# Kernel tuning notes

Measured on AMD Instinct MI355X. Metric: run time of the kernel, lower is better.

## Reference

```python
import jax, jax.numpy as jnp
import numpy as np

B, T, HID = 2, 2048, 2048
N_HEADS, N_KV, HEAD_DIM = 32, 8, 64
THETA = 10000.0
SCALE = HEAD_DIM ** -0.5
STEPS = 2  # entries already in cache before this call (step_idx)


def _rope_cos_sin(pos):
    # pos: [B, T] int -> cos/sin [B, T, HEAD_DIM]
    inv_freq = 1.0 / (THETA ** (jnp.arange(0, HEAD_DIM, 2, dtype=jnp.float32) / HEAD_DIM))
    freqs = pos.astype(jnp.float32)[..., None] * inv_freq  # [B,T,D/2]
    emb = jnp.concatenate([freqs, freqs], axis=-1)
    return jnp.cos(emb), jnp.sin(emb)


def _rotate_half(x):
    x1, x2 = jnp.split(x, 2, axis=-1)
    return jnp.concatenate([-x2, x1], axis=-1)


def setup_inputs() -> dict:
    key = jax.random.key(0)
    ks = jax.random.split(key, 8)
    combined_states = jax.random.normal(ks[0], (B, T, 2 * HID), dtype=jnp.float32)
    # additive causal mask: 0 on/below diagonal, large negative above
    causal = jnp.tril(jnp.ones((T, T), dtype=bool))
    attention_mask = jnp.where(causal, 0.0, -1e9).astype(jnp.float32)[None, None].repeat(B, axis=0)
    position_ids = jnp.broadcast_to(jnp.arange(T, dtype=jnp.int32), (B, T))
    prev_k = jax.random.normal(ks[1], (STEPS, B, N_HEADS, T, HEAD_DIM), dtype=jnp.float32)
    prev_v = jax.random.normal(ks[2], (STEPS, B, N_HEADS, T, HEAD_DIM), dtype=jnp.float32)
    Wq = 0.02 * jax.random.normal(ks[3], (2 * HID, N_HEADS * HEAD_DIM), dtype=jnp.float32)
    Wk = 0.02 * jax.random.normal(ks[4], (2 * HID, N_KV * HEAD_DIM), dtype=jnp.float32)
    Wv = 0.02 * jax.random.normal(ks[5], (2 * HID, N_KV * HEAD_DIM), dtype=jnp.float32)
    Wo = 0.02 * jax.random.normal(ks[6], (N_HEADS * HEAD_DIM, HID), dtype=jnp.float32)
    return {"combined_states": combined_states, "attention_mask": attention_mask,
            "position_ids": position_ids, "prev_k": prev_k, "prev_v": prev_v,
            "Wq": Wq, "Wk": Wk, "Wv": Wv, "Wo": Wo}


def reference(combined_states, attention_mask, position_ids, prev_k, prev_v, Wq, Wk, Wv, Wo):
    b, t, _ = combined_states.shape
    step_idx = prev_k.shape[0]  # len(cache_k) before append
    groups = N_HEADS // N_KV

    # fused QKV projection -> [B, H, T, D]
    q = (combined_states @ Wq).reshape(b, t, N_HEADS, HEAD_DIM).transpose(0, 2, 1, 3)
    k = (combined_states @ Wk).reshape(b, t, N_KV, HEAD_DIM).transpose(0, 2, 1, 3)
    v = (combined_states @ Wv).reshape(b, t, N_KV, HEAD_DIM).transpose(0, 2, 1, 3)

    # RoPE with phase shift by step_idx
    cos, sin = _rope_cos_sin(position_ids + step_idx)
    cos, sin = cos[:, None], sin[:, None]  # [B,1,T,D]
    q = q * cos + _rotate_half(q) * sin
    k = k * cos + _rotate_half(k) * sin

    # GQA expansion (repeat_interleave over head dim)
    k = jnp.repeat(k, groups, axis=1)
    v = jnp.repeat(v, groups, axis=1)

    # cache after append: [prev_0, prev_1, ..., k_new]; k0 = cache[0], later = cache[1:]
    k0, v0 = prev_k[0], prev_v[0]
    later_k = jnp.concatenate([prev_k[1:], k[None]], axis=0)  # [S, B, H, T, D], S = step_idx
    later_v = jnp.concatenate([prev_v[1:], v[None]], axis=0)

    # block attention over K_0 plus growing diagonal terms
    attn = jnp.einsum('bhtd,bhsd->bhts', q, k0) * SCALE + attention_mask  # [B,H,T,T]
    diag = jnp.einsum('bhtd,sbhtd->bhts', q, later_k) * SCALE             # [B,H,T,S]
    logits = jnp.concatenate([attn, diag], axis=-1)                        # [B,H,T,T+S]
    probs = jax.nn.softmax(logits.astype(jnp.float32), axis=-1).astype(q.dtype)

    out = jnp.einsum('bhts,bhsd->bhtd', probs[..., :t], v0)
    out = out + jnp.einsum('bhts,sbhtd->bhtd', probs[..., t:], later_v)
    out = out.transpose(0, 2, 1, 3).reshape(b, t, N_HEADS * HEAD_DIM)
    return out @ Wo
```

## Files before the change

### kernel.cpp

```cpp
#include <hip/hip_runtime.h>

#define B_    2
#define T_    2048
#define HID_  2048
#define NH_   32
#define NKV_  8
#define HD_   64
#define STEPS_ 2
#define SCALE_ 0.125f
#define CSC_  0.18033688011112042f

typedef float   f32x4  __attribute__((ext_vector_type(4)));
typedef __bf16  bf16x8 __attribute__((ext_vector_type(8)));
typedef unsigned short u16x8 __attribute__((ext_vector_type(8)));

__device__ __forceinline__ unsigned short f2bf(float f) {
  unsigned int u = __builtin_bit_cast(unsigned int, f);
  u = (u + 0x7fffu + ((u >> 16) & 1u)) >> 16;
  return (unsigned short)u;
}
__device__ __forceinline__ float bf2f(unsigned short h) {
  unsigned int u = ((unsigned int)h) << 16;
  return __builtin_bit_cast(float, u);
}
__device__ __forceinline__ bf16x8 frag_ld(const unsigned short* p) {
  u16x8 v = *(const u16x8*)p;
  return __builtin_bit_cast(bf16x8, v);
}
__device__ __forceinline__ f32x4 mfma16(bf16x8 a, bf16x8 b, f32x4 c) {
  return __builtin_amdgcn_mfma_f32_16x16x32_bf16(a, b, c, 0, 0, 0);
}
__device__ __forceinline__ void async_cp16(const void* g, void* l) {
  __builtin_amdgcn_global_load_lds(
      (const __attribute__((address_space(1))) void*)g,
      (__attribute__((address_space(3))) void*)l, 16, 0, 0);
}
__device__ __forceinline__ unsigned int cvtpk_bf16(float lo, float hi) {
  unsigned int r;
  asm("v_cvt_pk_bf16_f32 %0, %1, %2" : "=v"(r) : "v"(lo), "v"(hi));
  return r;
}

__global__ __launch_bounds__(256) void convert_bf16(const float* __restrict__ in,
                                                    unsigned short* __restrict__ out,
                                                    int n4) {
  int idx = blockIdx.x * 256 + threadIdx.x;
  if (idx < n4) {
    float4 v = ((const float4*)in)[idx];
    ushort4 o;
    o.x = f2bf(v.x); o.y = f2bf(v.y); o.z = f2bf(v.z); o.w = f2bf(v.w);
    ((ushort4*)out)[idx] = o;
  }
}

__global__ __launch_bounds__(256) void transpose_f32_bf16_ld(const float* __restrict__ in,
                                                             unsigned short* __restrict__ out,
                                                             int K, int N, int ldo) {
  __shared__ float tile[64][65];
  int n0 = blockIdx.x * 64, k0 = blockIdx.y * 64;
  int c = threadIdx.x & 63, w = threadIdx.x >> 6;
#pragma unroll
  for (int i = 0; i < 16; i++) {
    int r = w * 16 + i;
    tile[r][c] = in[(size_t)(k0 + r) * N + n0 + c];
  }
  __syncthreads();
#pragma unroll
  for (int i = 0; i < 16; i++) {
    int rr = w * 16 + i;
    out[(size_t)(n0 + rr) * ldo + k0 + c] = f2bf(tile[c][rr]);
  }
}

__global__ __launch_bounds__(256) void transpose_v0(const float* __restrict__ v0,
                                                    unsigned short* __restrict__ v0t) {
  __shared__ float tile[64][65];
  int s0 = blockIdx.x * 64;
  int bh = blockIdx.y;
  const float* src = v0 + (size_t)bh * T_ * HD_;
  unsigned short* dst = v0t + (size_t)bh * HD_ * T_;
  int c = threadIdx.x & 63, w = threadIdx.x >> 6;
#pragma unroll
  for (int i = 0; i < 16; i++) {
    int r = w * 16 + i;
    tile[r][c] = src[(size_t)(s0 + r) * HD_ + c];
  }
  __syncthreads();
#pragma unroll
  for (int i = 0; i < 16; i++) {
    int rr = w * 16 + i;
    dst[(size_t)rr * T_ + s0 + c] = f2bf(tile[c][rr]);
  }
}

#define SBAR  do { __builtin_amdgcn_sched_barrier(0); __builtin_amdgcn_s_barrier(); \
                   __builtin_amdgcn_sched_barrier(0); } while (0)
#define LGKM0 do { asm volatile("s_waitcnt lgkmcnt(0)" ::: "memory"); \
                   __builtin_amdgcn_sched_barrier(0); } while (0)
#define VM2   do { asm volatile("s_waitcnt vmcnt(2)" ::: "memory"); } while (0)
#define VM0   do { asm volatile("s_waitcnt vmcnt(0)" ::: "memory"); } while (0)

template <int NF>
__global__ __launch_bounds__(512, 2) void gemm128_bt(const unsigned short* __restrict__ A,
                                                     const unsigned short* __restrict__ Bt,
                                                     float* __restrict__ C,
                                                     int M, int N, int K) {
  constexpr int NHF = NF / 2;
  constexpr int BROWS = 128 + NF * 64;
  __shared__ __attribute__((aligned(128))) unsigned short smem[2][BROWS * 64];

  const int tid  = threadIdx.x;
  const int lane = tid & 63;
  const int wid  = tid >> 6;
  const int wr   = wid >> 2;
  const int wc   = wid & 3;
  const int la   = lane & 15;
  const int lq   = lane >> 4;
  const int sw   = la & 7;
  const int m0   = blockIdx.x * 128;
  const int n0   = blockIdx.y * (NF * 64);

  const int sr = lane >> 3;
  const int sl = (lane & 7) ^ sr;

  const unsigned short* gA[2];
  const unsigned short* gB[NHF][2];
#pragma unroll
  for (int is = 0; is < 2; ++is) {
    int r = (wid * 2 + is) * 8 + sr;
    gA[is] = A + (size_t)(m0 + r) * K + sl * 8;
#pragma unroll
    for (int u = 0; u < NHF; ++u)
      gB[u][is] = Bt + (size_t)(n0 + u * 128 + r) * K + sl * 8;
  }

#define G_STG_A(buf, kt) do { \
    async_cp16(gA[0] + (size_t)(kt) * 64, &smem[buf][(wid * 2 + 0) * 512]); \
    async_cp16(gA[1] + (size_t)(kt) * 64, &smem[buf][(wid * 2 + 1) * 512]); \
  } while (0)
#define G_STG_B(buf, u, kt) do { \
    async_cp16(gB[u][0] + (size_t)(kt) * 64, &smem[buf][(128 + (u) * 128) * 64 + (wid * 2 + 0) * 512]); \
    async_cp16(gB[u][1] + (size_t)(kt) * 64, &smem[buf][(128 + (u) * 128) * 64 + (wid * 2 + 1) * 512]); \
  } while (0)

  f32x4  acc[4][NF] = {};
  bf16x8 aR[2][2], b0r[NHF][2], b1r[NHF][2];

#define G_RD_A(buf, qm) do { \
    const unsigned short* rp_ = &smem[buf][0]; \
    _Pragma("unroll") \
    for (int i_ = 0; i_ < 2; ++i_) { \
      int ro_ = (wr * 64 + (qm) * 32 + i_ * 16 + la) * 64; \
      aR[i_][0] = frag_ld(rp_ + ro_ + (((0 + lq) ^ sw) << 3)); \
      aR[i_][1] = frag_ld(rp_ + ro_ + (((4 + lq) ^ sw) << 3)); \
    } \
  } while (0)
#define G_RD_B(buf, qn, breg) do { \
    const unsigned short* rp_ = &smem[buf][128 * 64]; \
    _Pragma("unroll") \
    for (int j_ = 0; j_ < NHF; ++j_) { \
      int ro_ = (wc * (NF * 16) + (qn) * (NF * 8) + j_ * 16 + la) * 64; \
      breg[j_][0] = frag_ld(rp_ + ro_ + (((0 + lq) ^ sw) << 3)); \
      breg[j_][1] = frag_ld(rp_ + ro_ + (((4 + lq) ^ sw) << 3)); \
    } \
  } while (0)
#define G_MMA(qm, qn, breg) do { \
    _Pragma("unroll") \
    for (int i_ = 0; i_ < 2; ++i_) \
      _Pragma("unroll") \
      for (int j_ = 0; j_ < NHF; ++j_) { \
        f32x4 c_ = acc[(qm) * 2 + i_][(qn) * NHF + j_]; \
        c_ = mfma16(aR[i_][0], breg[j_][0], c_); \
        c_ = mfma16(aR[i_][1], breg[j_][1], c_); \
        acc[(qm) * 2 + i_][(qn) * NHF + j_] = c_; \
      } \
  } while (0)

  G_STG_A(0, 0);
#pragma unroll
  for (int u = 0; u < NHF; ++u) G_STG_B(0, u, 0);
  if constexpr (NF == 6) G_STG_B(1, 2, 1); else G_STG_A(1, 1);
  VM2;
  SBAR;

  const int NI = K >> 7;
  for (int it = 0; it < NI; ++it) {
    const int e = it * 2;
    const bool pf = (it + 1 < NI);
    G_RD_A(0, 0);
    G_RD_B(0, 0, b0r);
    if constexpr (NF == 6) G_STG_A(1, e + 1); else G_STG_B(1, 0, e + 1);
    SBAR; LGKM0;
    __builtin_amdgcn_s_setprio(1); G_MMA(0, 0, b0r); __builtin_amdgcn_s_setprio(0);
    SBAR;
    G_RD_B(0, 1, b1r);
    if constexpr (NF == 6) G_STG_B(1, 0, e + 1); else G_STG_B(1, 1, e + 1);
    SBAR; LGKM0;
    __builtin_amdgcn_s_setprio(1); G_MMA(0, 1, b1r); __builtin_amdgcn_s_setprio(0);
    SBAR;
    G_RD_A(0, 1);
    if constexpr (NF == 6) G_STG_B(1, 1, e + 1);
    SBAR; LGKM0;
    __builtin_amdgcn_s_setprio(1); G_MMA(1, 1, b1r); __builtin_amdgcn_s_setprio(0);
    SBAR;
    if (pf) G_STG_A(0, e + 2);
    SBAR; LGKM0;
    __builtin_amdgcn_s_setprio(1); G_MMA(1, 0, b0r); __builtin_amdgcn_s_setprio(0);
    if (pf) { VM2; } else { VM0; }
    SBAR;
    G_RD_A(1, 0);
    G_RD_B(1, 0, b0r);
    if (pf) G_STG_B(0, 0, e + 2);
    SBAR; LGKM0;
    __builtin_amdgcn_s_setprio(1); G_MMA(0, 0, b0r); __builtin_amdgcn_s_setprio(0);
    SBAR;
    G_RD_B(1, 1, b1r);
    if (pf) G_STG_B(0, 1, e + 2);
    SBAR; LGKM0;
    __builtin_amdgcn_s_setprio(1); G_MMA(0, 1, b1r); __builtin_amdgcn_s_setprio(0);
    SBAR;
    G_RD_A(1, 1);
    if constexpr (NF == 6) { if (pf) G_STG_B(0, 2, e + 2); }
    SBAR; LGKM0;
    __builtin_amdgcn_s_setprio(1); G_MMA(1, 1, b1r); __builtin_amdgcn_s_setprio(0);
    SBAR;
    if constexpr (NF == 6) { if (pf) G_STG_B(1, 2, e + 3); }
    else                   { if (pf) G_STG_A(1, e + 3); }
    SBAR; LGKM0;
    __builtin_amdgcn_s_setprio(1); G_MMA(1, 0, b0r); __builtin_amdgcn_s_setprio(0);
    VM2;
    SBAR;
  }

#pragma unroll
  for (int mf = 0; mf < 4; ++mf) {
    int row = m0 + wr * 64 + mf * 16 + lq * 4;
#pragma unroll
    for (int nf = 0; nf < NF; ++nf) {
      int col = n0 + wc * (NF * 16) + nf * 16 + la;
#pragma unroll
      for (int r = 0; r < 4; ++r)
        C[(size_t)(row + r) * N + col] = acc[mf][nf][r];
    }
  }
#undef G_STG_A
#undef G_STG_B
#undef G_RD_A
#undef G_RD_B
#undef G_MMA
}

__global__ __launch_bounds__(256) void rope_kernel(const float* __restrict__ QKV,
                                                   const int* __restrict__ pos_ids,
                                                   unsigned short* __restrict__ q_b,
                                                   float* __restrict__ knew) {
  int idx = blockIdx.x * 256 + threadIdx.x;
  const int total = B_ * T_ * (NH_ + NKV_) * 32;
  if (idx >= total) return;
  int i = idx & 31;
  int tmp = idx >> 5;
  int hh = tmp % (NH_ + NKV_);
  int bt = tmp / (NH_ + NKV_);
  int t = bt & (T_ - 1);
  int b = bt >> 11;
  int pos = pos_ids[bt] + STEPS_;
  float inv = exp2f(-(float)i * (13.287712379549449f / 32.0f));
  float ang = (float)pos * inv;
  float sn, cs;
  sincosf(ang, &sn, &cs);
  const float* rowp = QKV + (size_t)bt * 3072;
  if (hh < NH_) {
    float x1 = rowp[hh * 64 + i];
    float x2 = rowp[hh * 64 + 32 + i];
    float y1 = (x1 * cs - x2 * sn) * CSC_;
    float y2 = (x2 * cs + x1 * sn) * CSC_;
    size_t o = ((size_t)(b * NH_ + hh) * T_ + t) * HD_ + i;
    q_b[o] = f2bf(y1);
    q_b[o + 32] = f2bf(y2);
  } else {
    int kv = hh - NH_;
    float x1 = rowp[2048 + kv * 64 + i];
    float x2 = rowp[2048 + kv * 64 + 32 + i];
    float y1 = x1 * cs - x2 * sn;
    float y2 = x2 * cs + x1 * sn;
    size_t o = ((size_t)(b * NKV_ + kv) * T_ + t) * HD_ + i;
    knew[o] = y1;
    knew[o + 32] = y2;
  }
}

__global__ __launch_bounds__(256, 3) void flash_kernel(const unsigned short* __restrict__ qb,
                                                       const unsigned short* __restrict__ k0b,
                                                       const unsigned short* __restrict__ v0t,
                                                       const float* __restrict__ prev_k,
                                                       const float* __restrict__ prev_v,
                                                       const float* __restrict__ knew,
                                                       const float* __restrict__ QKV,
                                                       unsigned short* __restrict__ attnout) {
  __shared__ unsigned short sK[2][64 * 64];
  __shared__ unsigned short sV[2][64 * 64];
  __shared__ unsigned short sP[4][2][16 * 72];

  const int tid = threadIdx.x;
  const int lane = tid & 63;
  const int wave = tid >> 6;
  const int la = lane & 15;
  const int lq = lane >> 4;
  const int swz = la & 7;

  const int id = blockIdx.x;
  const int bh = (id & 7) * 8 + ((id >> 3) & 7);
  const int qt = 15 - (id >> 6);

  const size_t bhs = (size_t)bh;
  const unsigned short* gK = k0b + bhs * T_ * HD_;
  const unsigned short* gV = v0t + bhs * HD_ * T_;

  const int rb0 = qt * 128 + wave * 32;
  const int ktd = rb0 >> 6;
  const int ktmax = 2 * qt + 1;

  bf16x8 aq[2][2];
#pragma unroll
  for (int f = 0; f < 2; f++) {
    const unsigned short* qp = qb + (bhs * T_ + rb0 + f * 16 + la) * HD_;
    aq[f][0] = frag_ld(qp + lq * 8);
    aq[f][1] = frag_ld(qp + 32 + lq * 8);
  }

  f32x4 o[2][4] = {};
  float m_f[2] = {-1e30f, -1e30f};
  float l_p[2] = {0.0f, 0.0f};

  const int lrow = lane >> 3;
  const int lcb = (lane & 7) ^ lrow;

  {
    unsigned short* kd = &sK[0][wave * 1024];
    unsigned short* vd = &sV[0][wave * 1024];
    async_cp16(gK + (size_t)(wave * 16 + lrow) * HD_ + lcb * 8, kd);
    async_cp16(gK + (size_t)(wave * 16 + 8 + lrow) * HD_ + lcb * 8, kd + 512);
    async_cp16(gV + (size_t)(wave * 16 + lrow) * T_ + lcb * 8, vd);
    async_cp16(gV + (size_t)(wave * 16 + 8 + lrow) * T_ + lcb * 8, vd + 512);
  }
  __syncthreads();

  int cur = 0;
  for (int kt = 0; kt <= ktmax; ++kt) {
    if (kt < ktmax) {
      const int nk = (kt + 1) * 64;
      unsigned short* kd = &sK[cur ^ 1][wave * 1024];
      unsigned short* vd = &sV[cur ^ 1][wave * 1024];
      async_cp16(gK + (size_t)(nk + wave * 16 + lrow) * HD_ + lcb * 8, kd);
      async_cp16(gK + (size_t)(nk + wave * 16 + 8 + lrow) * HD_ + lcb * 8, kd + 512);
      async_cp16(gV + (size_t)(wave * 16 + lrow) * T_ + nk + lcb * 8, vd);
      async_cp16(gV + (size_t)(wave * 16 + 8 + lrow) * T_ + nk + lcb * 8, vd + 512);
    }

    if (kt <= ktd) {
      const unsigned short* kb = &sK[cur][0];
      const unsigned short* vb = &sV[cur][0];

      bf16x8 bk0[4], bk1[4];
#pragma unroll
      for (int nb = 0; nb < 4; nb++) {
        const unsigned short* rp = kb + (nb * 16 + la) * 64;
        bk0[nb] = frag_ld(rp + ((lq ^ swz) << 3));
        bk1[nb] = frag_ld(rp + (((lq + 4) ^ swz) << 3));
      }
      f32x4 s[2][4];
      __builtin_amdgcn_s_setprio(1);
#pragma unroll
      for (int f = 0; f < 2; f++)
#pragma unroll
        for (int nb = 0; nb < 4; nb++) {
          f32x4 z = {0.f, 0.f, 0.f, 0.f};
          z = mfma16(bk0[nb], aq[f][0], z);
          z = mfma16(bk1[nb], aq[f][1], z);
          s[f][nb] = z;
        }
      __builtin_amdgcn_s_setprio(0);

      bf16x8 bv0[4], bv1[4];
#pragma unroll
      for (int jd = 0; jd < 4; jd++) {
        const unsigned short* rp = vb + (jd * 16 + la) * 64;
        bv0[jd] = frag_ld(rp + ((lq ^ swz) << 3));
        bv1[jd] = frag_ld(rp + (((lq + 4) ^ swz) << 3));
      }

      const bool diag = (kt == ktd);
#pragma unroll
      for (int f = 0; f < 2; f++) {
        const int qrow = rb0 + f * 16 + la;
        if (diag) {
#pragma unroll
          for (int nb = 0; nb < 4; nb++)
#pragma unroll
            for (int r = 0; r < 4; r++) {
              int key = kt * 64 + nb * 16 + lq * 4 + r;
              s[f][nb][r] = (key <= qrow) ? s[f][nb][r] : -1e30f;
            }
        }
        float t0 = fmaxf(fmaxf(s[f][0][0], s[f][0][1]), fmaxf(s[f][0][2], s[f][0][3]));
        float t1 = fmaxf(fmaxf(s[f][1][0], s[f][1][1]), fmaxf(s[f][1][2], s[f][1][3]));
        float t2 = fmaxf(fmaxf(s[f][2][0], s[f][2][1]), fmaxf(s[f][2][2], s[f][2][3]));
        float t3 = fmaxf(fmaxf(s[f][3][0], s[f][3][1]), fmaxf(s[f][3][2], s[f][3][3]));
        float tm = fmaxf(fmaxf(t0, t1), fmaxf(t2, t3));
        const bool resc = __any(tm > m_f[f] + 8.0f);
        if (resc) {
          tm = fmaxf(tm, __shfl_xor(tm, 16));
          tm = fmaxf(tm, __shfl_xor(tm, 32));
          float mn = fmaxf(m_f[f], tm);
          float al = exp2f(m_f[f] - mn);
          m_f[f] = mn;
          l_p[f] *= al;
          float a0 = __shfl(al, lq * 4 + 0);
          float a1 = __shfl(al, lq * 4 + 1);
          float a2 = __shfl(al, lq * 4 + 2);
          float a3 = __shfl(al, lq * 4 + 3);
#pragma unroll
          for (int jd = 0; jd < 4; jd++) {
            o[f][jd][0] *= a0;
            o[f][jd][1] *= a1;
            o[f][jd][2] *= a2;
            o[f][jd][3] *= a3;
          }
        }
        float ls = 0.0f;
#pragma unroll
        for (int nb = 0; nb < 4; nb++)
#pragma unroll
          for (int r = 0; r < 4; r++) {
            float p = exp2f(s[f][nb][r] - m_f[f]);
            s[f][nb][r] = p;
            ls += p;
          }
        l_p[f] += ls;
        unsigned short* pw = &sP[wave][f][0];
#pragma unroll
        for (int nb = 0; nb < 4; nb++) {
          unsigned int p01 = cvtpk_bf16(s[f][nb][0], s[f][nb][1]);
          unsigned int p23 = cvtpk_bf16(s[f][nb][2], s[f][nb][3]);
          unsigned long long pq = ((unsigned long long)p23 << 32) | (unsigned long long)p01;
          *(unsigned long long*)(pw + la * 72 + nb * 16 + lq * 4) = pq;
        }
      }

#pragma unroll
      for (int f = 0; f < 2; f++) {
        const unsigned short* pr = &sP[wave][f][0];
        bf16x8 ap0 = frag_ld(&pr[la * 72 + lq * 8]);
        bf16x8 ap1 = frag_ld(&pr[la * 72 + 32 + lq * 8]);
        __builtin_amdgcn_s_setprio(1);
#pragma unroll
        for (int jd = 0; jd < 4; jd++) {
          o[f][jd] = mfma16(ap0, bv0[jd], o[f][jd]);
          o[f][jd] = mfma16(ap1, bv1[jd], o[f][jd]);
        }
        __builtin_amdgcn_s_setprio(0);
      }
    }
    __syncthreads();
    cur ^= 1;
  }

#pragma unroll
  for (int f = 0; f < 2; f++) {
    l_p[f] += __shfl_xor(l_p[f], 16);
    l_p[f] += __shfl_xor(l_p[f], 32);
  }

  const int bI = bh >> 5;
  const int hI = bh & 31;
  const int kvI = hI >> 2;
  const size_t P1 = (size_t)B_ * NH_ * T_ * HD_;
  const float* k1base = prev_k + P1 + bhs * T_ * HD_;
  const float* v1base = prev_v + P1 + bhs * T_ * HD_;
  const float* knbase = knew + ((size_t)bI * NKV_ + kvI) * T_ * HD_;
  const float* vnbase = QKV + (size_t)bI * T_ * 3072 + 2560 + kvI * 64;
  unsigned short* aobase = attnout + (size_t)bI * T_ * (NH_ * HD_) + hI * HD_;

#pragma unroll
  for (int f = 0; f < 2; f++) {
    const int rowA = rb0 + f * 16 + la;
    const float* k1p = k1base + (size_t)rowA * HD_;
    const float* knp = knbase + (size_t)rowA * HD_;
    float e1 = 0.f, e2 = 0.f;
#pragma unroll
    for (int h2 = 0; h2 < 2; h2++) {
      const int dd = h2 * 32 + lq * 8;
#pragma unroll
      for (int j = 0; j < 8; j++) {
        float qv = (float)aq[f][h2][j];
        e1 = fmaf(qv, k1p[dd + j], e1);
        e2 = fmaf(qv, knp[dd + j], e2);
      }
    }
    e1 += __shfl_xor(e1, 16); e1 += __shfl_xor(e1, 32);
    e2 += __shfl_xor(e2, 16); e2 += __shfl_xor(e2, 32);
    float mx = fmaxf(m_f[f], fmaxf(e1, e2));
    float w0 = exp2f(m_f[f] - mx);
    float w1 = exp2f(e1 - mx);
    float w2 = exp2f(e2 - mx);
    float inv = 1.0f / (l_p[f] * w0 + w1 + w2);
    float s0 = w0 * inv, s1 = w1 * inv, s2 = w2 * inv;
    float a0[4], a1[4], a2[4];
#pragma unroll
    for (int r = 0; r < 4; r++) {
      a0[r] = __shfl(s0, lq * 4 + r);
      a1[r] = __shfl(s1, lq * 4 + r);
      a2[r] = __shfl(s2, lq * 4 + r);
    }
#pragma unroll
    for (int r = 0; r < 4; r++) {
      const int rowO = rb0 + f * 16 + lq * 4 + r;
      const float* v1p = v1base + (size_t)rowO * HD_;
      const float* vnp = vnbase + (size_t)rowO * 3072;
      unsigned short* aop = aobase + (size_t)rowO * (NH_ * HD_);
#pragma unroll
      for (int jd = 0; jd < 4; jd++) {
        int d = jd * 16 + la;
        float out = o[f][jd][r] * a0[r] + v1p[d] * a1[r] + vnp[d] * a2[r];
        aop[d] = f2bf(out);
      }
    }
  }
}

#define OFF_QKV   ((size_t)0)
#define OFF_XB    ((size_t)50331648)
#define OFF_WQKVT ((size_t)83886080)
#define OFF_WOT   ((size_t)109051904)
#define OFF_QB    ((size_t)117440512)
#define OFF_K0B   ((size_t)134217728)
#define OFF_V0T   ((size_t)150994944)
#define OFF_KNEW  ((size_t)167772160)
#define OFF_ML    ((size_t)176160768)

extern "C" void kernel_launch(void* const* d_in, const int* in_sizes, int n_in,
                              void* d_out, int out_size, void* d_ws, size_t ws_size,
                              hipStream_t stream) {
  const float* X = (const float*)d_in[0];
  const int* pos = (const int*)d_in[2];
  const float* prevk = (const float*)d_in[3];
  const float* prevv = (const float*)d_in[4];
  const float* Wq = (const float*)d_in[5];
  const float* Wk = (const float*)d_in[6];
  const float* Wv = (const float*)d_in[7];
  const float* Wo = (const float*)d_in[8];

  char* ws = (char*)d_ws;
  float* QKV = (float*)(ws + OFF_QKV);
  unsigned short* Xb = (unsigned short*)(ws + OFF_XB);
  unsigned short* WqkvT = (unsigned short*)(ws + OFF_WQKVT);
  unsigned short* attnout = (unsigned short*)(ws + OFF_WQKVT);
  unsigned short* WoT = (unsigned short*)(ws + OFF_WOT);
  unsigned short* q_b = (unsigned short*)(ws + OFF_QB);
  unsigned short* k0b = (unsigned short*)(ws + OFF_K0B);
  unsigned short* v0t = (unsigned short*)(ws + OFF_V0T);
  float* knew = (float*)(ws + OFF_KNEW);

  convert_bf16<<<16384, 256, 0, stream>>>(X, Xb, 4194304);
  transpose_f32_bf16_ld<<<dim3(32, 64), 256, 0, stream>>>(Wq, WqkvT, 4096, 2048, 4096);
  transpose_f32_bf16_ld<<<dim3(8, 64), 256, 0, stream>>>(Wk, WqkvT + (size_t)2048 * 4096, 4096, 512, 4096);
  transpose_f32_bf16_ld<<<dim3(8, 64), 256, 0, stream>>>(Wv, WqkvT + (size_t)2560 * 4096, 4096, 512, 4096);
  transpose_f32_bf16_ld<<<dim3(32, 32), 256, 0, stream>>>(Wo, WoT, 2048, 2048, 2048);
  convert_bf16<<<8192, 256, 0, stream>>>(prevk, k0b, 2097152);
  transpose_v0<<<dim3(32, 64), 256, 0, stream>>>(prevv, v0t);

  gemm128_bt<6><<<dim3(32, 8), 512, 0, stream>>>(Xb, WqkvT, QKV, 4096, 3072, 4096);

  rope_kernel<<<20480, 256, 0, stream>>>(QKV, pos, q_b, knew);

  flash_kernel<<<1024, 256, 0, stream>>>(q_b, k0b, v0t, prevk, prevv, knew, QKV, attnout);

  gemm128_bt<4><<<dim3(32, 8), 512, 0, stream>>>(attnout, WoT, (float*)d_out, 4096, 2048, 2048);
}
```

Baseline: 503.1 us.

## Merge seven preprocessing kernels into one launch with wider transpose tiles

Replaces the separate bf16 conversion and weight/V0 transpose kernels with a single preproc kernel that dispatches on block index ranges. Transpose tiles grow to 128x64 and stores pack two bf16 values into one 32-bit write. This removes six launch gaps and tail effects and improves store width. In exchange the small conversion blocks carry a larger LDS allocation, which may reduce occupancy for them.

```diff
diff --git a/kernel.cpp b/kernel.cpp
--- a/kernel.cpp
+++ b/kernel.cpp
@@ -41,55 +41,78 @@
   return r;
 }
 
-__global__ __launch_bounds__(256) void convert_bf16(const float* __restrict__ in,
-                                                    unsigned short* __restrict__ out,
-                                                    int n4) {
-  int idx = blockIdx.x * 256 + threadIdx.x;
-  if (idx < n4) {
-    float4 v = ((const float4*)in)[idx];
+__global__ __launch_bounds__(256) void preproc(const float* __restrict__ X,
+                                               const float* __restrict__ prevk,
+                                               const float* __restrict__ prevv,
+                                               const float* __restrict__ Wq,
+                                               const float* __restrict__ Wk,
+                                               const float* __restrict__ Wv,
+                                               const float* __restrict__ Wo,
+                                               unsigned short* __restrict__ Xb,
+                                               unsigned short* __restrict__ k0b,
+                                               unsigned short* __restrict__ WqkvT,
+                                               unsigned short* __restrict__ WoT,
+                                               unsigned short* __restrict__ v0t) {
+  __shared__ float tile[128][65];
+  const int tid = threadIdx.x;
+  int blk = blockIdx.x;
+
+  if (blk < 16384) {
+    int idx = blk * 256 + tid;
+    float4 v = ((const float4*)X)[idx];
     ushort4 o;
     o.x = f2bf(v.x); o.y = f2bf(v.y); o.z = f2bf(v.z); o.w = f2bf(v.w);
-    ((ushort4*)out)[idx] = o;
-  }
-}
-
-__global__ __launch_bounds__(256) void transpose_f32_bf16_ld(const float* __restrict__ in,
-                                                             unsigned short* __restrict__ out,
-                                                             int K, int N, int ldo) {
-  __shared__ float tile[64][65];
-  int n0 = blockIdx.x * 64, k0 = blockIdx.y * 64;
-  int c = threadIdx.x & 63, w = threadIdx.x >> 6;
-#pragma unroll
-  for (int i = 0; i < 16; i++) {
-    int r = w * 16 + i;
+    ((ushort4*)Xb)[idx] = o;
+    return;
+  }
+  blk -= 16384;
+  if (blk < 8192) {
+    int idx = blk * 256 + tid;
+    float4 v = ((const float4*)prevk)[idx];
+    ushort4 o;
+    o.x = f2bf(v.x); o.y = f2bf(v.y); o.z = f2bf(v.z); o.w = f2bf(v.w);
+    ((ushort4*)k0b)[idx] = o;
+    return;
+  }
+  blk -= 8192;
+
+  const float* in;
+  unsigned short* out;
+  int N, ldo, k0, n0;
+  if (blk < 1536) {
+    int nt = blk % 48, kt = blk / 48;
+    k0 = kt * 128;
+    ldo = 4096;
+    if (nt < 32)      { in = Wq; N = 2048; out = WqkvT;                         n0 = nt * 64; }
+    else if (nt < 40) { in = Wk; N = 512;  out = WqkvT + (size_t)2048 * 4096;   n0 = (nt - 32) * 64; }
+    else              { in = Wv; N = 512;  out = WqkvT + (size_t)2560 * 4096;   n0 = (nt - 40) * 64; }
+  } else if (blk < 2048) {
+    int q = blk - 1536;
+    int nt = q % 32, kt = q / 32;
+    in = Wo; out = WoT; N = 2048; ldo = 2048;
+    k0 = kt * 128; n0 = nt * 64;
+  } else {
+    int q = blk - 2048;
+    int st = q % 16, bh = q / 16;
+    in = prevv + (size_t)bh * T_ * HD_;
+    out = v0t + (size_t)bh * HD_ * T_;
+    N = 64; ldo = T_;
+    k0 = st * 128; n0 = 0;
+  }
+
+  const int c = tid & 63, w = tid >> 6;
+#pragma unroll
+  for (int i = 0; i < 32; i++) {
+    int r = w * 32 + i;
     tile[r][c] = in[(size_t)(k0 + r) * N + n0 + c];
   }
   __syncthreads();
 #pragma unroll
-  for (int i = 0; i < 16; i++) {
-    int rr = w * 16 + i;
-    out[(size_t)(n0 + rr) * ldo + k0 + c] = f2bf(tile[c][rr]);
-  }
-}
-
-__global__ __launch_bounds__(256) void transpose_v0(const float* __restrict__ v0,
-                                                    unsigned short* __restrict__ v0t) {
-  __shared__ float tile[64][65];
-  int s0 = blockIdx.x * 64;
-  int bh = blockIdx.y;
-  const float* src = v0 + (size_t)bh * T_ * HD_;
-  unsigned short* dst = v0t + (size_t)bh * HD_ * T_;
-  int c = threadIdx.x & 63, w = threadIdx.x >> 6;
-#pragma unroll
-  for (int i = 0; i < 16; i++) {
-    int r = w * 16 + i;
-    tile[r][c] = src[(size_t)(s0 + r) * HD_ + c];
-  }
-  __syncthreads();
-#pragma unroll
-  for (int i = 0; i < 16; i++) {
-    int rr = w * 16 + i;
-    dst[(size_t)rr * T_ + s0 + c] = f2bf(tile[c][rr]);
+  for (int ii = 0; ii < 16; ii++) {
+    int rr = w * 16 + ii;
+    unsigned int u = (unsigned int)f2bf(tile[c * 2][rr]) |
+                     ((unsigned int)f2bf(tile[c * 2 + 1][rr]) << 16);
+    *(unsigned int*)&out[(size_t)(n0 + rr) * ldo + k0 + c * 2] = u;
   }
 }
 
@@ -561,13 +584,8 @@
   unsigned short* v0t = (unsigned short*)(ws + OFF_V0T);
   float* knew = (float*)(ws + OFF_KNEW);
 
-  convert_bf16<<<16384, 256, 0, stream>>>(X, Xb, 4194304);
-  transpose_f32_bf16_ld<<<dim3(32, 64), 256, 0, stream>>>(Wq, WqkvT, 4096, 2048, 4096);
-  transpose_f32_bf16_ld<<<dim3(8, 64), 256, 0, stream>>>(Wk, WqkvT + (size_t)2048 * 4096, 4096, 512, 4096);
-  transpose_f32_bf16_ld<<<dim3(8, 64), 256, 0, stream>>>(Wv, WqkvT + (size_t)2560 * 4096, 4096, 512, 4096);
-  transpose_f32_bf16_ld<<<dim3(32, 32), 256, 0, stream>>>(Wo, WoT, 2048, 2048, 2048);
-  convert_bf16<<<8192, 256, 0, stream>>>(prevk, k0b, 2097152);
-  transpose_v0<<<dim3(32, 64), 256, 0, stream>>>(prevv, v0t);
+  preproc<<<27648, 256, 0, stream>>>(X, prevk, prevv, Wq, Wk, Wv, Wo,
+                                     Xb, k0b, WqkvT, WoT, v0t);
 
   gemm128_bt<6><<<dim3(32, 8), 512, 0, stream>>>(Xb, WqkvT, QKV, 4096, 3072, 4096);
 
```

Measured after the change: 494.7 us (median of 2 runs). Within noise of the previous version (-1.7%).
